# Performance work log

Measured on AMD Instinct MI355X. Metric: run time of the kernel, lower is better.

The kernel has to match this reference:

```python
import jax, jax.numpy as jnp
import numpy as np

N = 50000   # number of nodes
E = 25000   # number of hyperedges
IN = 256
OUT = 256
L = 32      # incidence list width (padded with 0)
NEG = -9e15  # matches torch's -9000000000000000.0 (fits in fp32)


def setup_inputs() -> dict:
    key = jax.random.key(0)
    k1, k2, k3, k4, k5 = jax.random.split(key, 5)
    x = jax.random.normal(k1, (N, IN), dtype=jnp.float32)
    seq = jax.random.randint(k2, (E, L), 0, N)      # node ids per hyperedge
    useq = jax.random.randint(k3, (N, L), 0, E)     # edge ids per node
    stdv = 1.0 / np.sqrt(IN)
    W1 = jax.random.uniform(k4, (IN, OUT), minval=-stdv, maxval=stdv, dtype=jnp.float32)
    W2 = jax.random.uniform(k5, (OUT, OUT), minval=-stdv, maxval=stdv, dtype=jnp.float32)
    return {"x": x, "seq": seq, "useq": useq, "W1": W1, "W2": W2}


def _mask_softmax_weights(idx):
    # softmax over where(idx>0, 1, -9e15): uniform weights over non-padding slots
    logits = jnp.where(idx > 0, 1.0, NEG).astype(jnp.float32)
    return jax.nn.softmax(logits, axis=1)


def reference(x, seq, useq, W1, W2):
    x1 = x @ W1                                   # [N, OUT]
    w = _mask_softmax_weights(seq)                # [E, L]
    edge = jnp.einsum('elc,el->ec', x1[seq], w)   # gather + weighted reduce -> [E, OUT]
    # F.dropout is identity in eval mode
    edge = jax.nn.relu(edge)
    e1 = edge @ W2                                # [E, OUT]
    uw = _mask_softmax_weights(useq)              # [N, L]
    node = jnp.einsum('nlc,nl->nc', e1[useq], uw) # [N, OUT]
    return node
```

## Files before the change

### kernel.cpp

```cpp
#include <hip/hip_runtime.h>

constexpr int N_NODES = 50000;
constexpr int N_EDGES = 25000;
constexpr int C = 256;
constexpr int L = 32;

__device__ ushort W1T_g[C * C];
__device__ ushort W2T_g[C * C];

__device__ __forceinline__ ushort f2bf(float f) {
    union { float f; unsigned int u; } c; c.f = f;
    unsigned int r = c.u + 0x7FFFu + ((c.u >> 16) & 1u);
    return (ushort)(r >> 16);
}
__device__ __forceinline__ float bflo(unsigned int u) {
    union { unsigned int x; float f; } c; c.x = u << 16; return c.f;
}
__device__ __forceinline__ float bfhi(unsigned int u) {
    union { unsigned int x; float f; } c; c.x = u & 0xFFFF0000u; return c.f;
}
__device__ __forceinline__ void acc_uint4(float* acc, const uint4 v) {
    acc[0] += bflo(v.x); acc[1] += bfhi(v.x);
    acc[2] += bflo(v.y); acc[3] += bfhi(v.y);
    acc[4] += bflo(v.z); acc[5] += bfhi(v.z);
    acc[6] += bflo(v.w); acc[7] += bfhi(v.w);
}

__global__ __launch_bounds__(256) void convert_x_kernel(
    const float* __restrict__ x, ushort* __restrict__ xb)
{
    const size_t i = ((size_t)blockIdx.x * 256 + threadIdx.x) * 4;
    const float4 v = *reinterpret_cast<const float4*>(x + i);
    ushort4 o;
    o.x = f2bf(v.x); o.y = f2bf(v.y); o.z = f2bf(v.z); o.w = f2bf(v.w);
    *reinterpret_cast<ushort4*>(xb + i) = o;
}

__global__ __launch_bounds__(256) void wconv_kernel(
    const float* __restrict__ W1, const float* __restrict__ W2)
{
    const float* W  = blockIdx.z ? W2 : W1;
    ushort* WT      = blockIdx.z ? W2T_g : W1T_g;
    __shared__ float t[64][65];
    const int rr = threadIdx.x >> 6;
    const int cc = threadIdx.x & 63;
    const int br = blockIdx.x * 64;
    const int bc = blockIdx.y * 64;
#pragma unroll
    for (int i = 0; i < 16; ++i) {
        const int row = i * 4 + rr;
        t[row][cc] = W[(size_t)(br + row) * C + bc + cc];
    }
    __syncthreads();
#pragma unroll
    for (int i = 0; i < 16; ++i) {
        const int n = i * 4 + rr;
        WT[(size_t)(bc + n) * C + br + cc] = f2bf(t[cc][n]);
    }
}

__global__ __launch_bounds__(256) void gather_edge_kernel(
    const ushort* __restrict__ src, const int* __restrict__ idx,
    ushort* __restrict__ dst, int nrows)
{
    const int row = blockIdx.x * 8 + (threadIdx.x >> 5);
    const int ln  = threadIdx.x & 31;
    if (row >= nrows) return;

    const int myid = idx[(size_t)row * L + ln];
    const unsigned long long b = __ballot(myid > 0);
    const unsigned int halfmask = (unsigned int)(b >> (threadIdx.x & 32));
    const int cnt = __popc(halfmask);

    float acc[8] = {0.f, 0.f, 0.f, 0.f, 0.f, 0.f, 0.f, 0.f};
#pragma unroll
    for (int l = 0; l < L; ++l) {
        const int id = __shfl(myid, l, 32);
        const uint4 v = *reinterpret_cast<const uint4*>(
            src + (size_t)id * C + ln * 8);
        acc_uint4(acc, v);
    }
    const uint4 v0 = *reinterpret_cast<const uint4*>(src + ln * 8);
    float x0[8];
    x0[0] = bflo(v0.x); x0[1] = bfhi(v0.x); x0[2] = bflo(v0.y); x0[3] = bfhi(v0.y);
    x0[4] = bflo(v0.z); x0[5] = bfhi(v0.z); x0[6] = bflo(v0.w); x0[7] = bfhi(v0.w);

    const float corr = (cnt == 0) ? 0.f : (float)(L - cnt);
    const float inv  = (cnt == 0) ? (1.f / (float)L) : (1.f / (float)cnt);

    ushort* d = dst + (size_t)row * C + ln * 8;
    uint4 o;
    o.x = (unsigned)f2bf((acc[0] - corr * x0[0]) * inv) |
          ((unsigned)f2bf((acc[1] - corr * x0[1]) * inv) << 16);
    o.y = (unsigned)f2bf((acc[2] - corr * x0[2]) * inv) |
          ((unsigned)f2bf((acc[3] - corr * x0[3]) * inv) << 16);
    o.z = (unsigned)f2bf((acc[4] - corr * x0[4]) * inv) |
          ((unsigned)f2bf((acc[5] - corr * x0[5]) * inv) << 16);
    o.w = (unsigned)f2bf((acc[6] - corr * x0[6]) * inv) |
          ((unsigned)f2bf((acc[7] - corr * x0[7]) * inv) << 16);
    *reinterpret_cast<uint4*>(d) = o;
}

__global__ __launch_bounds__(256) void gather_node_kernel(
    const ushort* __restrict__ src, const int* __restrict__ idx,
    float* __restrict__ dst, int nrows)
{
    constexpr int CH = 64, NCHUNK = 4;
    constexpr int LPR = CH / 8;
    constexpr int RPB = 256 / LPR;
    const int chunk = blockIdx.x & (NCHUNK - 1);
    const int rb    = (int)(blockIdx.x / NCHUNK) * RPB;
    const int t     = threadIdx.x;

    __shared__ int sidx[RPB][33];
#pragma unroll
    for (int i = 0; i < (RPB * L) / 256; ++i) {
        const int flat = i * 256 + t;
        const int r = flat >> 5, l = flat & 31;
        sidx[r][l] = (rb + r < nrows) ? idx[(size_t)(rb + r) * L + l] : 0;
    }
    __syncthreads();

    const int r   = t / LPR;
    const int ch  = chunk * CH + (t % LPR) * 8;
    const int row = rb + r;
    if (row >= nrows) return;

    float acc[8] = {0.f, 0.f, 0.f, 0.f, 0.f, 0.f, 0.f, 0.f};
    int cnt = 0;
#pragma unroll
    for (int l = 0; l < L; ++l) {
        const int id = sidx[r][l];
        cnt += (id > 0) ? 1 : 0;
        const uint4 v = *reinterpret_cast<const uint4*>(
            src + (size_t)id * C + ch);
        acc_uint4(acc, v);
    }
    const uint4 v0 = *reinterpret_cast<const uint4*>(src + ch);
    float x0[8];
    x0[0] = bflo(v0.x); x0[1] = bfhi(v0.x); x0[2] = bflo(v0.y); x0[3] = bfhi(v0.y);
    x0[4] = bflo(v0.z); x0[5] = bfhi(v0.z); x0[6] = bflo(v0.w); x0[7] = bfhi(v0.w);

    const float corr = (cnt == 0) ? 0.f : (float)(L - cnt);
    const float inv  = (cnt == 0) ? (1.f / (float)L) : (1.f / (float)cnt);

    float* d = dst + (size_t)row * C + ch;
    float4 o0 = {(acc[0] - corr * x0[0]) * inv, (acc[1] - corr * x0[1]) * inv,
                 (acc[2] - corr * x0[2]) * inv, (acc[3] - corr * x0[3]) * inv};
    float4 o1 = {(acc[4] - corr * x0[4]) * inv, (acc[5] - corr * x0[5]) * inv,
                 (acc[6] - corr * x0[6]) * inv, (acc[7] - corr * x0[7]) * inv};
    *reinterpret_cast<float4*>(d)     = o0;
    *reinterpret_cast<float4*>(d + 4) = o1;
}

typedef __attribute__((ext_vector_type(8))) short bf16x8;
typedef __attribute__((ext_vector_type(4))) float f32x4;

template <bool RELU>
__global__ __launch_bounds__(256) void gemm_mfma_kernel(
    const ushort* __restrict__ A, int which_w,
    ushort* __restrict__ Cmat, int M)
{
    const ushort* __restrict__ BT = which_w ? W2T_g : W1T_g;
    const int wave  = threadIdx.x >> 6;
    const int lane  = threadIdx.x & 63;
    const int quad  = lane >> 4;
    const int l16   = lane & 15;
    const int base  = (blockIdx.x * 4 + wave) * 32;
    const int nbase = blockIdx.y * 128;

    int m0 = base + l16;      if (m0 > M - 1) m0 = M - 1;
    int m1 = base + 16 + l16; if (m1 > M - 1) m1 = M - 1;

    f32x4 acc[2][8];
    const f32x4 zero = {0.f, 0.f, 0.f, 0.f};
#pragma unroll
    for (int p = 0; p < 2; ++p)
#pragma unroll
        for (int t = 0; t < 8; ++t) acc[p][t] = zero;

    const ushort* a0 = A + (size_t)m0 * C + quad * 8;
    const ushort* a1 = A + (size_t)m1 * C + quad * 8;
    const ushort* br = BT + (size_t)(nbase + l16) * C + quad * 8;

#pragma unroll
    for (int k0 = 0; k0 < C; k0 += 32) {
        const bf16x8 av0 = *reinterpret_cast<const bf16x8*>(a0 + k0);
        const bf16x8 av1 = *reinterpret_cast<const bf16x8*>(a1 + k0);
#pragma unroll
        for (int t = 0; t < 8; ++t) {
            const bf16x8 b = *reinterpret_cast<const bf16x8*>(
                br + (size_t)t * 16 * C + k0);
            acc[0][t] = __builtin_amdgcn_mfma_f32_16x16x32_bf16(av0, b, acc[0][t], 0, 0, 0);
            acc[1][t] = __builtin_amdgcn_mfma_f32_16x16x32_bf16(av1, b, acc[1][t], 0, 0, 0);
        }
    }

#pragma unroll
    for (int p = 0; p < 2; ++p)
#pragma unroll
    for (int t = 0; t < 8; ++t)
#pragma unroll
    for (int r = 0; r < 4; ++r) {
        const int gm = base + p * 16 + quad * 4 + r;
        if (gm < M) {
            float v = acc[p][t][r];
            if (RELU) v = fmaxf(v, 0.f);
            Cmat[(size_t)gm * C + nbase + t * 16 + l16] = f2bf(v);
        }
    }
}

extern "C" void kernel_launch(void* const* d_in, const int* in_sizes, int n_in,
                              void* d_out, int out_size, void* d_ws, size_t ws_size,
                              hipStream_t stream) {
    const float* x    = (const float*)d_in[0];
    const int*   seq  = (const int*)d_in[1];
    const int*   useq = (const int*)d_in[2];
    const float* W1   = (const float*)d_in[3];
    const float* W2   = (const float*)d_in[4];
    float* out = (float*)d_out;

    ushort* xb   = (ushort*)d_ws;
    ushort* tmp1 = xb + (size_t)N_NODES * C;
    ushort* edge = tmp1 + (size_t)N_EDGES * C;

    convert_x_kernel<<<dim3((N_NODES * C) / (256 * 4)), dim3(256), 0, stream>>>(x, xb);
    wconv_kernel<<<dim3(4, 4, 2), dim3(256), 0, stream>>>(W1, W2);

    gather_edge_kernel<<<dim3((N_EDGES + 7) / 8), dim3(256), 0, stream>>>(
        xb, seq, tmp1, N_EDGES);

    const dim3 ggrid((N_EDGES + 127) / 128, 2);
    gemm_mfma_kernel<true><<<ggrid, dim3(256), 0, stream>>>(tmp1, 0, edge, N_EDGES);
    gemm_mfma_kernel<false><<<ggrid, dim3(256), 0, stream>>>(edge, 1, tmp1, N_EDGES);

    const int rblk2 = (N_NODES + 31) / 32;
    gather_node_kernel<<<dim3(4 * rblk2), dim3(256), 0, stream>>>(
        tmp1, useq, out, N_NODES);
}
```

Before: 280.5 us.

## Reorder W2 projection after node gather and use zero-row padding in gathers

```diff
diff --git a/kernel.cpp b/kernel.cpp
--- a/kernel.cpp
+++ b/kernel.cpp
@@ -34,6 +34,15 @@
     ushort4 o;
     o.x = f2bf(v.x); o.y = f2bf(v.y); o.z = f2bf(v.z); o.w = f2bf(v.w);
     *reinterpret_cast<ushort4*>(xb + i) = o;
+}
+
+__global__ __launch_bounds__(64) void zrow_kernel(
+    ushort* __restrict__ xb_zrow, ushort* __restrict__ edge_zrow)
+{
+    const int t = threadIdx.x;
+    const uint4 z = {0u, 0u, 0u, 0u};
+    if (t < 32) reinterpret_cast<uint4*>(xb_zrow)[t] = z;
+    else        reinterpret_cast<uint4*>(edge_zrow)[t - 32] = z;
 }
 
 __global__ __launch_bounds__(256) void wconv_kernel(
@@ -59,51 +68,9 @@
     }
 }
 
-__global__ __launch_bounds__(256) void gather_edge_kernel(
+__global__ __launch_bounds__(256, 6) void gather_chunk_kernel(
     const ushort* __restrict__ src, const int* __restrict__ idx,
-    ushort* __restrict__ dst, int nrows)
-{
-    const int row = blockIdx.x * 8 + (threadIdx.x >> 5);
-    const int ln  = threadIdx.x & 31;
-    if (row >= nrows) return;
-
-    const int myid = idx[(size_t)row * L + ln];
-    const unsigned long long b = __ballot(myid > 0);
-    const unsigned int halfmask = (unsigned int)(b >> (threadIdx.x & 32));
-    const int cnt = __popc(halfmask);
-
-    float acc[8] = {0.f, 0.f, 0.f, 0.f, 0.f, 0.f, 0.f, 0.f};
-#pragma unroll
-    for (int l = 0; l < L; ++l) {
-        const int id = __shfl(myid, l, 32);
-        const uint4 v = *reinterpret_cast<const uint4*>(
-            src + (size_t)id * C + ln * 8);
-        acc_uint4(acc, v);
-    }
-    const uint4 v0 = *reinterpret_cast<const uint4*>(src + ln * 8);
-    float x0[8];
-    x0[0] = bflo(v0.x); x0[1] = bfhi(v0.x); x0[2] = bflo(v0.y); x0[3] = bfhi(v0.y);
-    x0[4] = bflo(v0.z); x0[5] = bfhi(v0.z); x0[6] = bflo(v0.w); x0[7] = bfhi(v0.w);
-
-    const float corr = (cnt == 0) ? 0.f : (float)(L - cnt);
-    const float inv  = (cnt == 0) ? (1.f / (float)L) : (1.f / (float)cnt);
-
-    ushort* d = dst + (size_t)row * C + ln * 8;
-    uint4 o;
-    o.x = (unsigned)f2bf((acc[0] - corr * x0[0]) * inv) |
-          ((unsigned)f2bf((acc[1] - corr * x0[1]) * inv) << 16);
-    o.y = (unsigned)f2bf((acc[2] - corr * x0[2]) * inv) |
-          ((unsigned)f2bf((acc[3] - corr * x0[3]) * inv) << 16);
-    o.z = (unsigned)f2bf((acc[4] - corr * x0[4]) * inv) |
-          ((unsigned)f2bf((acc[5] - corr * x0[5]) * inv) << 16);
-    o.w = (unsigned)f2bf((acc[6] - corr * x0[6]) * inv) |
-          ((unsigned)f2bf((acc[7] - corr * x0[7]) * inv) << 16);
-    *reinterpret_cast<uint4*>(d) = o;
-}
-
-__global__ __launch_bounds__(256) void gather_node_kernel(
-    const ushort* __restrict__ src, const int* __restrict__ idx,
-    float* __restrict__ dst, int nrows)
+    ushort* __restrict__ dst, int nrows, int zrow)
 {
     constexpr int CH = 64, NCHUNK = 4;
     constexpr int LPR = CH / 8;
@@ -117,49 +84,51 @@
     for (int i = 0; i < (RPB * L) / 256; ++i) {
         const int flat = i * 256 + t;
         const int r = flat >> 5, l = flat & 31;
-        sidx[r][l] = (rb + r < nrows) ? idx[(size_t)(rb + r) * L + l] : 0;
+        int raw = (rb + r < nrows) ? idx[(size_t)(rb + r) * L + l] : 0;
+        sidx[r][l] = (raw > 0) ? raw : zrow;
     }
     __syncthreads();
 
     const int r   = t / LPR;
     const int ch  = chunk * CH + (t % LPR) * 8;
     const int row = rb + r;
-    if (row >= nrows) return;
 
     float acc[8] = {0.f, 0.f, 0.f, 0.f, 0.f, 0.f, 0.f, 0.f};
     int cnt = 0;
 #pragma unroll
     for (int l = 0; l < L; ++l) {
         const int id = sidx[r][l];
-        cnt += (id > 0) ? 1 : 0;
+        cnt += (id != zrow) ? 1 : 0;
         const uint4 v = *reinterpret_cast<const uint4*>(
             src + (size_t)id * C + ch);
         acc_uint4(acc, v);
     }
-    const uint4 v0 = *reinterpret_cast<const uint4*>(src + ch);
-    float x0[8];
-    x0[0] = bflo(v0.x); x0[1] = bfhi(v0.x); x0[2] = bflo(v0.y); x0[3] = bfhi(v0.y);
-    x0[4] = bflo(v0.z); x0[5] = bfhi(v0.z); x0[6] = bflo(v0.w); x0[7] = bfhi(v0.w);
-
-    const float corr = (cnt == 0) ? 0.f : (float)(L - cnt);
-    const float inv  = (cnt == 0) ? (1.f / (float)L) : (1.f / (float)cnt);
-
-    float* d = dst + (size_t)row * C + ch;
-    float4 o0 = {(acc[0] - corr * x0[0]) * inv, (acc[1] - corr * x0[1]) * inv,
-                 (acc[2] - corr * x0[2]) * inv, (acc[3] - corr * x0[3]) * inv};
-    float4 o1 = {(acc[4] - corr * x0[4]) * inv, (acc[5] - corr * x0[5]) * inv,
-                 (acc[6] - corr * x0[6]) * inv, (acc[7] - corr * x0[7]) * inv};
-    *reinterpret_cast<float4*>(d)     = o0;
-    *reinterpret_cast<float4*>(d + 4) = o1;
+    if (row >= nrows) return;
+
+    float inv;
+    if (cnt == 0) {
+        const uint4 v = *reinterpret_cast<const uint4*>(src + ch);
+        acc[0] = bflo(v.x); acc[1] = bfhi(v.x); acc[2] = bflo(v.y); acc[3] = bfhi(v.y);
+        acc[4] = bflo(v.z); acc[5] = bfhi(v.z); acc[6] = bflo(v.w); acc[7] = bfhi(v.w);
+        inv = 1.f;
+    } else {
+        inv = 1.f / (float)cnt;
+    }
+
+    uint4 o;
+    o.x = (unsigned)f2bf(acc[0] * inv) | ((unsigned)f2bf(acc[1] * inv) << 16);
+    o.y = (unsigned)f2bf(acc[2] * inv) | ((unsigned)f2bf(acc[3] * inv) << 16);
+    o.z = (unsigned)f2bf(acc[4] * inv) | ((unsigned)f2bf(acc[5] * inv) << 16);
+    o.w = (unsigned)f2bf(acc[6] * inv) | ((unsigned)f2bf(acc[7] * inv) << 16);
+    *reinterpret_cast<uint4*>(dst + (size_t)row * C + ch) = o;
 }
 
 typedef __attribute__((ext_vector_type(8))) short bf16x8;
 typedef __attribute__((ext_vector_type(4))) float f32x4;
 
-template <bool RELU>
+template <bool RELU, bool F32OUT>
 __global__ __launch_bounds__(256) void gemm_mfma_kernel(
-    const ushort* __restrict__ A, int which_w,
-    ushort* __restrict__ Cmat, int M)
+    const ushort* __restrict__ A, int which_w, void* __restrict__ Cmat, int M)
 {
     const ushort* __restrict__ BT = which_w ? W2T_g : W1T_g;
     const int wave  = threadIdx.x >> 6;
@@ -206,7 +175,10 @@
         if (gm < M) {
             float v = acc[p][t][r];
             if (RELU) v = fmaxf(v, 0.f);
-            Cmat[(size_t)gm * C + nbase + t * 16 + l16] = f2bf(v);
+            if (F32OUT)
+                ((float*)Cmat)[(size_t)gm * C + nbase + t * 16 + l16] = v;
+            else
+                ((ushort*)Cmat)[(size_t)gm * C + nbase + t * 16 + l16] = f2bf(v);
         }
     }
 }
@@ -222,20 +194,24 @@
     float* out = (float*)d_out;
 
     ushort* xb   = (ushort*)d_ws;
-    ushort* tmp1 = xb + (size_t)N_NODES * C;
+    ushort* tmp1 = xb + (size_t)(N_NODES + 1) * C;
     ushort* edge = tmp1 + (size_t)N_EDGES * C;
+    ushort* agg  = xb;
 
     convert_x_kernel<<<dim3((N_NODES * C) / (256 * 4)), dim3(256), 0, stream>>>(x, xb);
+    zrow_kernel<<<dim3(1), dim3(64), 0, stream>>>(
+        xb + (size_t)N_NODES * C, edge + (size_t)N_EDGES * C);
     wconv_kernel<<<dim3(4, 4, 2), dim3(256), 0, stream>>>(W1, W2);
 
-    gather_edge_kernel<<<dim3((N_EDGES + 7) / 8), dim3(256), 0, stream>>>(
-        xb, seq, tmp1, N_EDGES);
-
-    const dim3 ggrid((N_EDGES + 127) / 128, 2);
-    gemm_mfma_kernel<true><<<ggrid, dim3(256), 0, stream>>>(tmp1, 0, edge, N_EDGES);
-    gemm_mfma_kernel<false><<<ggrid, dim3(256), 0, stream>>>(edge, 1, tmp1, N_EDGES);
-
-    const int rblk2 = (N_NODES + 31) / 32;
-    gather_node_kernel<<<dim3(4 * rblk2), dim3(256), 0, stream>>>(
-        tmp1, useq, out, N_NODES);
-}
+    gather_chunk_kernel<<<dim3(4 * ((N_EDGES + 31) / 32)), dim3(256), 0, stream>>>(
+        xb, seq, tmp1, N_EDGES, N_NODES);
+
+    gemm_mfma_kernel<true, false><<<dim3((N_EDGES + 127) / 128, 2), dim3(256), 0, stream>>>(
+        tmp1, 0, edge, N_EDGES);
+
+    gather_chunk_kernel<<<dim3(4 * ((N_NODES + 31) / 32)), dim3(256), 0, stream>>>(
+        edge, useq, agg, N_NODES, N_EDGES);
+
+    gemm_mfma_kernel<false, true><<<dim3((N_NODES + 127) / 128, 2), dim3(256), 0, stream>>>(
+        agg, 1, out, N_NODES);
+}
```

Result: slower. 646.7 us (+130.6%).
